# Kernel tuning notes

Hardware: AMD Instinct MI355X
Metric: run time of the kernel (lower is better)

## Reference

```python
import jax, jax.numpy as jnp
import numpy as np

IN, H, FC1, FC2, OUT = 3, 30, 64, 32, 1
B, T = 8192, 256


def _lstm_layer(xT, W_ih, W_hh, b_ih, b_hh):
    """xT: (T, B, Din). Returns (hidden sequence (T,B,H), final h (B,H)).
    PyTorch gate order: i, f, g, o."""
    # Precompute input contribution for all timesteps (one big GEMM).
    gx = jnp.einsum('tbd,gd->tbg', xT, W_ih) + b_ih + b_hh  # (T,B,4H)
    b = xT.shape[1]
    h0 = jnp.zeros((b, W_hh.shape[1]), xT.dtype)
    c0 = h0

    def step(carry, g):
        h, c = carry
        gates = g + h @ W_hh.T
        i, f, gg, o = jnp.split(gates, 4, axis=-1)
        i = jax.nn.sigmoid(i)
        f = jax.nn.sigmoid(f)
        gg = jnp.tanh(gg)
        o = jax.nn.sigmoid(o)
        c = f * c + i * gg
        h = o * jnp.tanh(c)
        return (h, c), h

    (h_n, _), ys = jax.lax.scan(step, (h0, c0), gx)
    return ys, h_n


def setup_inputs() -> dict:
    key = jax.random.key(0)
    ks = jax.random.split(key, 16)
    s = 0.18  # ~1/sqrt(hidden_size), matches PyTorch uniform init scale
    inp = {
        'x': jax.random.normal(ks[0], (B, T, IN), jnp.float32),
        'W_ih0': jax.random.normal(ks[1], (4 * H, IN), jnp.float32) * s,
        'W_hh0': jax.random.normal(ks[2], (4 * H, H), jnp.float32) * s,
        'b_ih0': jax.random.normal(ks[3], (4 * H,), jnp.float32) * s,
        'b_hh0': jax.random.normal(ks[4], (4 * H,), jnp.float32) * s,
        'W_ih1': jax.random.normal(ks[5], (4 * H, H), jnp.float32) * s,
        'W_hh1': jax.random.normal(ks[6], (4 * H, H), jnp.float32) * s,
        'b_ih1': jax.random.normal(ks[7], (4 * H,), jnp.float32) * s,
        'b_hh1': jax.random.normal(ks[8], (4 * H,), jnp.float32) * s,
        'W_fc1': jax.random.normal(ks[9], (FC1, H), jnp.float32) * s,
        'b_fc1': jax.random.normal(ks[10], (FC1,), jnp.float32) * s,
        'W_fc2': jax.random.normal(ks[11], (FC2, FC1), jnp.float32) * 0.125,
        'b_fc2': jax.random.normal(ks[12], (FC2,), jnp.float32) * 0.125,
        'W_fc3': jax.random.normal(ks[13], (OUT, FC2), jnp.float32) * 0.17,
        'b_fc3': jax.random.normal(ks[14], (OUT,), jnp.float32) * 0.17,
    }
    return inp


def reference(x, W_ih0, W_hh0, b_ih0, b_hh0, W_ih1, W_hh1, b_ih1, b_hh1,
              W_fc1, b_fc1, W_fc2, b_fc2, W_fc3, b_fc3):
    xT = jnp.swapaxes(x, 0, 1)  # (T,B,IN)
    ys, _ = _lstm_layer(xT, W_ih0, W_hh0, b_ih0, b_hh0)   # layer 0 sequence
    _, h_n = _lstm_layer(ys, W_ih1, W_hh1, b_ih1, b_hh1)  # layer 1 final h
    # FC head (dropout = identity in eval mode)
    z = jax.nn.relu(h_n @ W_fc1.T + b_fc1)
    z = jax.nn.relu(z @ W_fc2.T + b_fc2)
    z = jax.nn.sigmoid(z @ W_fc3.T + b_fc3)
    return z.squeeze(-1)  # (B,)
```

## Files before the change

### kernel.cpp

```cpp
#include <hip/hip_runtime.h>

#define TT   256
#define HID  30
#define LOG2E 1.4426950408889634f
#define HS   56
#define XW   772

typedef __bf16 bf16x8_t __attribute__((ext_vector_type(8)));
typedef float  f32x4_t  __attribute__((ext_vector_type(4)));

__device__ __forceinline__ float fexp2(float x){
#if __has_builtin(__builtin_amdgcn_exp2f)
    return __builtin_amdgcn_exp2f(x);
#else
    return exp2f(x);
#endif
}
__device__ __forceinline__ float frcp(float x){
#if __has_builtin(__builtin_amdgcn_rcpf)
    return __builtin_amdgcn_rcpf(x);
#else
    return 1.f/x;
#endif
}
__device__ __forceinline__ float fsigmoid(float x){ return frcp(1.f + fexp2(-LOG2E*x)); }
__device__ __forceinline__ f32x4_t exp4(f32x4_t v){
    f32x4_t e; e[0]=fexp2(v[0]); e[1]=fexp2(v[1]); e[2]=fexp2(v[2]); e[3]=fexp2(v[3]); return e;
}
__device__ __forceinline__ f32x4_t rcp4(f32x4_t v){
    f32x4_t r; r[0]=frcp(v[0]); r[1]=frcp(v[1]); r[2]=frcp(v[2]); r[3]=frcp(v[3]); return r;
}
__device__ __forceinline__ f32x4_t sig4(f32x4_t v){ return rcp4(exp4(v*(-LOG2E)) + 1.f); }
__device__ __forceinline__ f32x4_t tanh4(f32x4_t v){ return rcp4(exp4(v*(-2.f*LOG2E)) + 1.f)*2.f - 1.f; }

#define MFMA(A,B,C) __builtin_amdgcn_mfma_f32_16x16x32_bf16(A,B,C,0,0,0)

__global__ __launch_bounds__(128)
void lstm_fused(const float* __restrict__ x,
    const float* __restrict__ Wih0, const float* __restrict__ Whh0,
    const float* __restrict__ bih0, const float* __restrict__ bhh0,
    const float* __restrict__ Wih1, const float* __restrict__ Whh1,
    const float* __restrict__ bih1, const float* __restrict__ bhh1,
    const float* __restrict__ Wfc1, const float* __restrict__ bfc1,
    const float* __restrict__ Wfc2, const float* __restrict__ bfc2,
    const float* __restrict__ Wfc3, const float* __restrict__ bfc3,
    float* __restrict__ out)
{
    __shared__ __align__(16) __bf16 h0f[2][16][HS];
    __shared__ __align__(16) __bf16 h1f[16][HS];
    __shared__ __align__(16) float  sx[16*XW];
    __shared__ float h1_last[16*32];
    __shared__ float zbuf[16*64];
    __shared__ float z2buf[16*32];

    const int tid  = threadIdx.x;
    const int lane = tid & 63;
    const int wv   = tid >> 6;
    const int n    = lane & 15;
    const int q    = lane >> 4;
    const int bbase = blockIdx.x * 16;

    {
        const float* xB = x + (size_t)bbase * 768;
        #pragma unroll
        for (int it = 0; it < 24; ++it) {
            int flat = (it*128 + tid) * 4;
            int m = flat / 768;
            int o = flat - m*768;
            const float4 v = *(const float4*)(xB + (size_t)m*768 + o);
            *(float4*)(&sx[m*XW + o]) = v;
        }
    }

    bf16x8_t fb0[8];
    bf16x8_t fb1[8];
    float bias[8], wx2v[8];
    #pragma unroll
    for (int t = 0; t < 8; ++t) {
        const int G = t >> 1;
        const int u = (t & 1)*16 + n;
        const bool ok = (u < HID);
        const int row = G*HID + (ok ? u : 0);
        #pragma unroll
        for (int j = 0; j < 8; ++j) {
            const int k = q*8 + j;
            float v0 = 0.f, v1 = 0.f;
            if (ok) {
                if (wv == 0) {
                    v0 = (k < HID) ? Whh0[row*HID + k] : Wih0[row*3 + (k - HID)];
                } else if (k < HID) {
                    v0 = Wih1[row*HID + k];
                    v1 = Whh1[row*HID + k];
                }
            }
            fb0[t][j] = (__bf16)v0;
            fb1[t][j] = (__bf16)v1;
        }
        bias[t] = ok ? (wv == 0 ? bih0[row] + bhh0[row] : bih1[row] + bhh1[row]) : 0.f;
        wx2v[t] = (ok && wv == 0) ? Wih0[row*3 + 2] : 0.f;
    }

    f32x4_t cA = {0.f,0.f,0.f,0.f};
    f32x4_t cB = {0.f,0.f,0.f,0.f};

    for (int i = tid; i < 2*16*HS; i += 128) (&h0f[0][0][0])[i] = (__bf16)0.f;
    for (int i = tid; i < 16*HS;   i += 128) (&h1f[0][0])[i]    = (__bf16)0.f;
    __syncthreads();
    if (tid < 32)
        h0f[1][tid>>1][30+(tid&1)] = (__bf16)sx[(tid>>1)*XW + (tid&1)];
    __syncthreads();

#define ACTS_AND_STATE(d)                                                    \
    f32x4_t i0 = sig4(d[0]),  i1 = sig4(d[1]);                               \
    f32x4_t f0 = sig4(d[2]),  f1 = sig4(d[3]);                               \
    f32x4_t g0 = tanh4(d[4]), g1 = tanh4(d[5]);                              \
    f32x4_t o0 = sig4(d[6]),  o1 = sig4(d[7]);                               \
    cA = f0*cA + i0*g0;                                                      \
    cB = f1*cB + i1*g1;                                                      \
    f32x4_t hA = o0*tanh4(cA);                                               \
    f32x4_t hB = o1*tanh4(cB);

#define STEP(S, RB, WB) do {                                                 \
    if (wv == 0) {                                                           \
        if ((S) + 1 < TT) {                            \
            bf16x8_t A0 = *(const bf16x8_t*)(&h0f[RB][n][q*8]);              \
            f32x4_t x2;                                                      \
            _Pragma("unroll")                                                \
            for (int r = 0; r < 4; ++r)                                      \
                x2[r] = sx[(q*4+r)*XW + ((S)+1)*3 + 2];                      \
            f32x4_t d[8];                                                    \
            _Pragma("unroll")                                                \
            for (int t = 0; t < 8; ++t) {                                    \
                f32x4_t cc = x2*wx2v[t] + bias[t];                           \
                d[t] = MFMA(A0, fb0[t], cc);                                 \
            }                                                                \
            ACTS_AND_STATE(d)                                                \
            _Pragma("unroll")                                                \
            for (int r = 0; r < 4; ++r) h0f[WB][q*4+r][n] = (__bf16)hA[r];   \
            if (n < 14) {                                                    \
                _Pragma("unroll")                                            \
                for (int r = 0; r < 4; ++r) h0f[WB][q*4+r][16+n] = (__bf16)hB[r]; \
            }                                                                \
        }                                                                    \
    } else {                                                                 \
               \
        {                                                                    \
            int tn = (S) + 2; if (tn > TT-1) tn = TT-1;                      \
            if (lane < 32) {                                                 \
                float xv = sx[(lane>>1)*XW + tn*3 + (lane&1)];               \
                h0f[WB][lane>>1][30+(lane&1)] = (__bf16)xv;                  \
            }                                                                \
        }                                                                    \
        if ((S) >= 0) {                                  \
            bf16x8_t A1 = *(const bf16x8_t*)(&h0f[RB][n][q*8]);              \
            bf16x8_t A2 = *(const bf16x8_t*)(&h1f[n][q*8]);                  \
            f32x4_t d[8];                                                    \
            _Pragma("unroll")                                                \
            for (int t = 0; t < 8; ++t) {                                    \
                f32x4_t cc = {bias[t], bias[t], bias[t], bias[t]};           \
                cc   = MFMA(A1, fb0[t], cc);                                 \
                d[t] = MFMA(A2, fb1[t], cc);                                 \
            }                                                                \
            ACTS_AND_STATE(d)                                                \
            _Pragma("unroll")                                                \
            for (int r = 0; r < 4; ++r) h1f[q*4+r][n] = (__bf16)hA[r];       \
            if (n < 14) {                                                    \
                _Pragma("unroll")                                            \
                for (int r = 0; r < 4; ++r) h1f[q*4+r][16+n] = (__bf16)hB[r]; \
            }                                                                \
            if ((S) == TT-1) {                                               \
                _Pragma("unroll")                                            \
                for (int r = 0; r < 4; ++r) {                                \
                    h1_last[(q*4+r)*32 + n] = hA[r];                         \
                    if (n < 14) h1_last[(q*4+r)*32 + 16+n] = hB[r];          \
                }                                                            \
            }                                                                \
        }                                                                    \
    }                                                                        \
    __syncthreads();                                                         \
} while (0)

    STEP(-1, 1, 0);
    #pragma unroll 1
    for (int s = 0; s < TT; s += 2) {
        STEP(s,   0, 1);
        STEP(s+1, 1, 0);
    }
#undef STEP
#undef ACTS_AND_STATE

    #pragma unroll
    for (int rep = 0; rep < 8; ++rep) {
        int idx = tid + rep*128;
        int m = idx >> 6, uu = idx & 63;
        float a = bfc1[uu];
        for (int k = 0; k < HID; ++k) a += h1_last[m*32+k] * Wfc1[uu*HID+k];
        zbuf[m*64+uu] = fmaxf(a, 0.f);
    }
    __syncthreads();
    #pragma unroll
    for (int rep = 0; rep < 4; ++rep) {
        int idx = tid + rep*128;
        int m = idx >> 5, v = idx & 31;
        float a = bfc2[v];
        for (int k = 0; k < 64; ++k) a += zbuf[m*64+k] * Wfc2[v*64+k];
        z2buf[m*32+v] = fmaxf(a, 0.f);
    }
    __syncthreads();
    if (tid < 16) {
        float a = bfc3[0];
        for (int k = 0; k < 32; ++k) a += z2buf[tid*32+k] * Wfc3[k];
        out[bbase + tid] = fsigmoid(a);
    }
}

extern "C" void kernel_launch(void* const* d_in, const int* in_sizes, int n_in,
                              void* d_out, int out_size, void* d_ws, size_t ws_size,
                              hipStream_t stream) {
    const float* x    = (const float*)d_in[0];
    const float* Wih0 = (const float*)d_in[1];
    const float* Whh0 = (const float*)d_in[2];
    const float* bih0 = (const float*)d_in[3];
    const float* bhh0 = (const float*)d_in[4];
    const float* Wih1 = (const float*)d_in[5];
    const float* Whh1 = (const float*)d_in[6];
    const float* bih1 = (const float*)d_in[7];
    const float* bhh1 = (const float*)d_in[8];
    const float* Wfc1 = (const float*)d_in[9];
    const float* bfc1 = (const float*)d_in[10];
    const float* Wfc2 = (const float*)d_in[11];
    const float* bfc2 = (const float*)d_in[12];
    const float* Wfc3 = (const float*)d_in[13];
    const float* bfc3 = (const float*)d_in[14];
    float* outp = (float*)d_out;

    hipLaunchKernelGGL(lstm_fused, dim3(512), dim3(128), 0, stream,
        x, Wih0, Whh0, bih0, bhh0, Wih1, Whh1, bih1, bhh1,
        Wfc1, bfc1, Wfc2, bfc2, Wfc3, bfc3, outp);
}
```

Before: 337.0 us.

## Batch four LSTM timesteps per barrier with triple-buffered layer-0 hidden ring

Layer-0 and layer-1 waves no longer synchronize every timestep. Wave 0 now computes four layer-0 steps into a chunk of a three-slot ring buffer, and wave 1 consumes the previous chunk, so there is one block barrier per four timesteps instead of one per step. The FC-head scratch buffers are also aliased onto the x staging area to cut LDS use, which may allow more resident blocks. The cost is more LDS for the hidden-state ring and more complex indexing. The two waves also now run a chunk apart, so layer 1 finishes later and runs a short tail after the loop.

```diff
diff --git a/kernel.cpp b/kernel.cpp
--- a/kernel.cpp
+++ b/kernel.cpp
@@ -46,12 +46,10 @@
     const float* __restrict__ Wfc3, const float* __restrict__ bfc3,
     float* __restrict__ out)
 {
-    __shared__ __align__(16) __bf16 h0f[2][16][HS];
+    __shared__ __align__(16) float  sx[16*XW];
+    __shared__ __align__(16) __bf16 h0r[3][4][16][HS];
     __shared__ __align__(16) __bf16 h1f[16][HS];
-    __shared__ __align__(16) float  sx[16*XW];
     __shared__ float h1_last[16*32];
-    __shared__ float zbuf[16*64];
-    __shared__ float z2buf[16*32];
 
     const int tid  = threadIdx.x;
     const int lane = tid & 63;
@@ -67,13 +65,11 @@
             int flat = (it*128 + tid) * 4;
             int m = flat / 768;
             int o = flat - m*768;
-            const float4 v = *(const float4*)(xB + (size_t)m*768 + o);
-            *(float4*)(&sx[m*XW + o]) = v;
+            *(float4*)(&sx[m*XW + o]) = *(const float4*)(xB + (size_t)m*768 + o);
         }
     }
 
-    bf16x8_t fb0[8];
-    bf16x8_t fb1[8];
+    bf16x8_t fbA[8], fbB[8];
     float bias[8], wx2v[8];
     #pragma unroll
     for (int t = 0; t < 8; ++t) {
@@ -84,17 +80,17 @@
         #pragma unroll
         for (int j = 0; j < 8; ++j) {
             const int k = q*8 + j;
-            float v0 = 0.f, v1 = 0.f;
+            float vA = 0.f, vB = 0.f;
             if (ok) {
                 if (wv == 0) {
-                    v0 = (k < HID) ? Whh0[row*HID + k] : Wih0[row*3 + (k - HID)];
+                    vA = (k < HID) ? Whh0[row*HID + k] : Wih0[row*3 + (k - HID)];
                 } else if (k < HID) {
-                    v0 = Wih1[row*HID + k];
-                    v1 = Whh1[row*HID + k];
+                    vA = Wih1[row*HID + k];
+                    vB = Whh1[row*HID + k];
                 }
             }
-            fb0[t][j] = (__bf16)v0;
-            fb1[t][j] = (__bf16)v1;
+            fbA[t][j] = (__bf16)vA;
+            fbB[t][j] = (__bf16)vB;
         }
         bias[t] = ok ? (wv == 0 ? bih0[row] + bhh0[row] : bih1[row] + bhh1[row]) : 0.f;
         wx2v[t] = (ok && wv == 0) ? Wih0[row*3 + 2] : 0.f;
@@ -103,14 +99,11 @@
     f32x4_t cA = {0.f,0.f,0.f,0.f};
     f32x4_t cB = {0.f,0.f,0.f,0.f};
 
-    for (int i = tid; i < 2*16*HS; i += 128) (&h0f[0][0][0])[i] = (__bf16)0.f;
-    for (int i = tid; i < 16*HS;   i += 128) (&h1f[0][0])[i]    = (__bf16)0.f;
-    __syncthreads();
-    if (tid < 32)
-        h0f[1][tid>>1][30+(tid&1)] = (__bf16)sx[(tid>>1)*XW + (tid&1)];
-    __syncthreads();
-
-#define ACTS_AND_STATE(d)                                                    \
+    for (int i = tid; i < 3*4*16*HS; i += 128) (&h0r[0][0][0][0])[i] = (__bf16)0.f;
+    for (int i = tid; i < 16*HS;     i += 128) (&h1f[0][0])[i]       = (__bf16)0.f;
+    __syncthreads();
+
+#define ACTS(d)                                                              \
     f32x4_t i0 = sig4(d[0]),  i1 = sig4(d[1]);                               \
     f32x4_t f0 = sig4(d[2]),  f1 = sig4(d[3]);                               \
     f32x4_t g0 = tanh4(d[4]), g1 = tanh4(d[5]);                              \
@@ -120,82 +113,114 @@
     f32x4_t hA = o0*tanh4(cA);                                               \
     f32x4_t hB = o1*tanh4(cB);
 
-#define STEP(S, RB, WB) do {                                                 \
-    if (wv == 0) {                                                           \
-        if ((S) + 1 < TT) {                            \
-            bf16x8_t A0 = *(const bf16x8_t*)(&h0f[RB][n][q*8]);              \
-            f32x4_t x2;                                                      \
-            _Pragma("unroll")                                                \
-            for (int r = 0; r < 4; ++r)                                      \
-                x2[r] = sx[(q*4+r)*XW + ((S)+1)*3 + 2];                      \
-            f32x4_t d[8];                                                    \
-            _Pragma("unroll")                                                \
-            for (int t = 0; t < 8; ++t) {                                    \
-                f32x4_t cc = x2*wx2v[t] + bias[t];                           \
-                d[t] = MFMA(A0, fb0[t], cc);                                 \
-            }                                                                \
-            ACTS_AND_STATE(d)                                                \
-            _Pragma("unroll")                                                \
-            for (int r = 0; r < 4; ++r) h0f[WB][q*4+r][n] = (__bf16)hA[r];   \
-            if (n < 14) {                                                    \
-                _Pragma("unroll")                                            \
-                for (int r = 0; r < 4; ++r) h0f[WB][q*4+r][16+n] = (__bf16)hB[r]; \
-            }                                                                \
+#define W0STEP(T, PR, JR, PW, JW) do {                                       \
+    bf16x8_t A0 = *(const bf16x8_t*)((PR) + ((JR)*16 + n)*HS + q*8);         \
+    f32x4_t x2;                                                              \
+    _Pragma("unroll")                                                        \
+    for (int r = 0; r < 4; ++r) x2[r] = sx[(q*4+r)*XW + (T)*3 + 2];          \
+    f32x4_t d[8];                                                            \
+    _Pragma("unroll")                                                        \
+    for (int t = 0; t < 8; ++t) d[t] = MFMA(A0, fbA[t], x2*wx2v[t]+bias[t]); \
+    ACTS(d)                                                                  \
+    __bf16* wp = (PW) + (JW)*16*HS;                                          \
+    _Pragma("unroll")                                                        \
+    for (int r = 0; r < 4; ++r) wp[(q*4+r)*HS + n] = (__bf16)hA[r];          \
+    if (n < 14) {                                                            \
+        _Pragma("unroll")                                                    \
+        for (int r = 0; r < 4; ++r) wp[(q*4+r)*HS + 16+n] = (__bf16)hB[r];   \
+    }                                                                        \
+    { int Tc = (T) + 1; if (Tc > TT-1) Tc = TT-1;                            \
+      if (lane < 32)                                                         \
+        wp[(lane>>1)*HS + 30 + (lane&1)] =                                   \
+            (__bf16)sx[(lane>>1)*XW + Tc*3 + (lane&1)]; }                    \
+} while (0)
+
+#define W1STEP(T, PR, JR) do {                                               \
+    bf16x8_t A1 = *(const bf16x8_t*)((PR) + ((JR)*16 + n)*HS + q*8);         \
+    bf16x8_t A2 = *(const bf16x8_t*)(&h1f[n][q*8]);                          \
+    f32x4_t d[8];                                                            \
+    _Pragma("unroll")                                                        \
+    for (int t = 0; t < 8; ++t) {                                            \
+        f32x4_t e = {bias[t], bias[t], bias[t], bias[t]};                    \
+        d[t] = MFMA(A1, fbA[t], e);                                          \
+    }                                                                        \
+    _Pragma("unroll")                                                        \
+    for (int t = 0; t < 8; ++t) d[t] = MFMA(A2, fbB[t], d[t]);               \
+    ACTS(d)                                                                  \
+    _Pragma("unroll")                                                        \
+    for (int r = 0; r < 4; ++r) h1f[q*4+r][n] = (__bf16)hA[r];               \
+    if (n < 14) {                                                            \
+        _Pragma("unroll")                                                    \
+        for (int r = 0; r < 4; ++r) h1f[q*4+r][16+n] = (__bf16)hB[r];        \
+    }                                                                        \
+    if ((T) == TT-1) {                                                       \
+        _Pragma("unroll")                                                    \
+        for (int r = 0; r < 4; ++r) {                                        \
+            h1_last[(q*4+r)*32 + n] = hA[r];                                 \
+            if (n < 14) h1_last[(q*4+r)*32 + 16+n] = hB[r];                  \
         }                                                                    \
-    } else {                                                                 \
-               \
-        {                                                                    \
-            int tn = (S) + 2; if (tn > TT-1) tn = TT-1;                      \
-            if (lane < 32) {                                                 \
-                float xv = sx[(lane>>1)*XW + tn*3 + (lane&1)];               \
-                h0f[WB][lane>>1][30+(lane&1)] = (__bf16)xv;                  \
-            }                                                                \
-        }                                                                    \
-        if ((S) >= 0) {                                  \
-            bf16x8_t A1 = *(const bf16x8_t*)(&h0f[RB][n][q*8]);              \
-            bf16x8_t A2 = *(const bf16x8_t*)(&h1f[n][q*8]);                  \
-            f32x4_t d[8];                                                    \
-            _Pragma("unroll")                                                \
-            for (int t = 0; t < 8; ++t) {                                    \
-                f32x4_t cc = {bias[t], bias[t], bias[t], bias[t]};           \
-                cc   = MFMA(A1, fb0[t], cc);                                 \
-                d[t] = MFMA(A2, fb1[t], cc);                                 \
-            }                                                                \
-            ACTS_AND_STATE(d)                                                \
-            _Pragma("unroll")                                                \
-            for (int r = 0; r < 4; ++r) h1f[q*4+r][n] = (__bf16)hA[r];       \
-            if (n < 14) {                                                    \
-                _Pragma("unroll")                                            \
-                for (int r = 0; r < 4; ++r) h1f[q*4+r][16+n] = (__bf16)hB[r]; \
-            }                                                                \
-            if ((S) == TT-1) {                                               \
-                _Pragma("unroll")                                            \
-                for (int r = 0; r < 4; ++r) {                                \
-                    h1_last[(q*4+r)*32 + n] = hA[r];                         \
-                    if (n < 14) h1_last[(q*4+r)*32 + 16+n] = hB[r];          \
-                }                                                            \
-            }                                                                \
-        }                                                                    \
-    }                                                                        \
-    __syncthreads();                                                         \
+    }                                                                        \
 } while (0)
 
-    STEP(-1, 1, 0);
+    if (wv == 0) {
+        if (lane < 32)
+            h0r[2][2][lane>>1][30+(lane&1)] = (__bf16)sx[(lane>>1)*XW + (lane&1)];
+        __bf16* b2 = &h0r[2][0][0][0];
+        W0STEP(0, b2, 2, b2, 3);
+    }
+    __syncthreads();
+
+    int kw = 0;
     #pragma unroll 1
-    for (int s = 0; s < TT; s += 2) {
-        STEP(s,   0, 1);
-        STEP(s+1, 1, 0);
-    }
-#undef STEP
-#undef ACTS_AND_STATE
+    for (int k = 0; k < 64; ++k) {
+        __bf16* bW = &h0r[kw][0][0][0];
+        const int kr = (kw == 0) ? 2 : kw - 1;
+        const __bf16* bR = &h0r[kr][0][0][0];
+        if (wv == 0) {
+            if (k < 63) {
+                const int T = 4*k;
+                W0STEP(T+1, bR, 3, bW, 0);
+                W0STEP(T+2, bW, 0, bW, 1);
+                W0STEP(T+3, bW, 1, bW, 2);
+                W0STEP(T+4, bW, 2, bW, 3);
+            } else {
+                W0STEP(253, bR, 3, bW, 0);
+                W0STEP(254, bW, 0, bW, 1);
+                W0STEP(255, bW, 1, bW, 2);
+            }
+        } else {
+            if (k == 0) {
+                W1STEP(0, bR, 3);
+            } else {
+                const int t0 = 4*k - 3;
+                W1STEP(t0,   bR, 0);
+                W1STEP(t0+1, bR, 1);
+                W1STEP(t0+2, bR, 2);
+                W1STEP(t0+3, bR, 3);
+            }
+        }
+        __syncthreads();
+        kw = (kw == 2) ? 0 : kw + 1;
+    }
+    if (wv == 1) {
+        const __bf16* bR = &h0r[0][0][0][0];
+        W1STEP(253, bR, 0);
+        W1STEP(254, bR, 1);
+        W1STEP(255, bR, 2);
+    }
+    __syncthreads();
+
+#undef W0STEP
+#undef W1STEP
+#undef ACTS
 
     #pragma unroll
     for (int rep = 0; rep < 8; ++rep) {
         int idx = tid + rep*128;
         int m = idx >> 6, uu = idx & 63;
         float a = bfc1[uu];
-        for (int k = 0; k < HID; ++k) a += h1_last[m*32+k] * Wfc1[uu*HID+k];
-        zbuf[m*64+uu] = fmaxf(a, 0.f);
+        for (int kk = 0; kk < HID; ++kk) a += h1_last[m*32+kk] * Wfc1[uu*HID+kk];
+        sx[m*64+uu] = fmaxf(a, 0.f);
     }
     __syncthreads();
     #pragma unroll
@@ -203,13 +228,13 @@
         int idx = tid + rep*128;
         int m = idx >> 5, v = idx & 31;
         float a = bfc2[v];
-        for (int k = 0; k < 64; ++k) a += zbuf[m*64+k] * Wfc2[v*64+k];
-        z2buf[m*32+v] = fmaxf(a, 0.f);
+        for (int kk = 0; kk < 64; ++kk) a += sx[m*64+kk] * Wfc2[v*64+kk];
+        sx[1024 + m*32+v] = fmaxf(a, 0.f);
     }
     __syncthreads();
     if (tid < 16) {
         float a = bfc3[0];
-        for (int k = 0; k < 32; ++k) a += z2buf[tid*32+k] * Wfc3[k];
+        for (int kk = 0; kk < 32; ++kk) a += sx[1024 + tid*32+kk] * Wfc3[kk];
         out[bbase + tid] = fsigmoid(a);
     }
 }
```

After: 350.9 us. 1.04x slower.
